# Kernel tuning notes

Measured on AMD Instinct MI355X. Metric: run time of the kernel, lower is better.

## Reference

```python
import jax, jax.numpy as jnp
import numpy as np

B, I, H = 8192, 1024, 1024


def setup_inputs() -> dict:
    key = jax.random.key(0)
    k1, k2, k3, k4, k5 = jax.random.split(key, 5)
    bound_in = 1.0 / np.sqrt(I)
    return {
        "input": jax.random.normal(k1, (B, I), dtype=jnp.float32),
        "weights": jax.random.uniform(k2, (4 * H, H + I), dtype=jnp.float32, minval=-bound_in, maxval=bound_in),
        "bias": jax.random.uniform(k3, (4 * H,), dtype=jnp.float32, minval=-bound_in, maxval=bound_in),
        "old_h": jax.random.normal(k4, (B, H), dtype=jnp.float32),
        "old_cell": jax.random.normal(k5, (B, H), dtype=jnp.float32),
    }


def reference(input, weights, bias, old_h, old_cell):
    # X = [old_h, input] matches weights = cat(recurrent_W, input_W, dim=1)
    X = jnp.concatenate([old_h, input], axis=1)            # [B, H+I]
    gates = jax.nn.sigmoid(X @ weights.T + bias)           # [B, 4H], all gates sigmoid
    in_g, out_g, z_g, f_g = jnp.split(gates, 4, axis=1)    # each [B, H]
    new_cell = old_cell * f_g + z_g - in_g                 # subtractive cell update
    new_h = jax.nn.sigmoid(new_cell) - out_g               # subtractive output
    return new_h, new_cell
```

## Files before the change

kernel.cpp:

```cpp
#include <hip/hip_runtime.h>
#include <hip/hip_bf16.h>

namespace {

constexpr int kB = 8192;
constexpr int kH = 1024;
constexpr int kK = 2048;
constexpr int kG = 4 * kH;

typedef float f32x4 __attribute__((ext_vector_type(4)));
typedef unsigned short u16x8 __attribute__((ext_vector_type(8)));
typedef unsigned short u16x4 __attribute__((ext_vector_type(4)));

__device__ __forceinline__ unsigned short f2bf(float f) {
  return __builtin_bit_cast(unsigned short, __float2bfloat16(f));
}
__device__ __forceinline__ float sigmoidf_(float x) {
  return 1.0f / (1.0f + __expf(-x));
}
__device__ __forceinline__ u16x4 pack4(const float4 v) {
  return u16x4{f2bf(v.x), f2bf(v.y), f2bf(v.z), f2bf(v.w)};
}

__global__ __launch_bounds__(256) void prep_pack(
    const float* __restrict__ input, const float* __restrict__ weights,
    const float* __restrict__ bias, const float* __restrict__ old_h,
    unsigned short* __restrict__ Aw, unsigned short* __restrict__ Ww,
    float* __restrict__ bias_i) {
  const int b = blockIdx.x;
  const int tid = threadIdx.x;

  if (b >= 768) {
    const int base = (b - 768) * 2048 + tid * 8;
    #pragma unroll
    for (int e = 0; e < 8; ++e) {
      const int j = base + e;
      bias_i[j] = bias[(j & 3) * kH + (j >> 2)];
    }
    return;
  }

  __shared__ unsigned short lbuf[128 * 280];

  const int wid = tid >> 6, lane = tid & 63;
  const bool isW = (b >= 512);
  const int blk = isW ? (b - 512) : b;
  const int rb = blk >> 3;
  const int kc = blk & 7;

  #pragma unroll
  for (int io = 0; io < 4; ++io) {
    float4 v[8];
    #pragma unroll
    for (int ii = 0; ii < 8; ++ii) {
      const int row = (io * 8 + ii) * 4 + wid;
      const float* base;
      if (!isW) {
        const long rowg = (long)rb * 128 + row;
        base = (kc < 4) ? (old_h + rowg * kH + kc * 256)
                        : (input + rowg * kH + (kc * 256 - kH));
      } else {
        const int j = rb * 128 + row;
        const int g = j & 3, h = j >> 2;
        base = weights + ((long)g * kH + h) * kK + kc * 256;
      }
      v[ii] = ((const float4*)base)[lane];
    }
    #pragma unroll
    for (int ii = 0; ii < 8; ++ii) {
      const int row = (io * 8 + ii) * 4 + wid;
      *(u16x4*)&lbuf[row * 280 + lane * 4] = pack4(v[ii]);
    }
  }
  __syncthreads();

  unsigned short* dst = (isW ? Ww : Aw) + ((long)rb * 32 + kc * 4) * 8192;
  #pragma unroll
  for (int it = 0; it < 16; ++it) {
    const int o = (it * 256 + tid) * 8;
    const int oo = o & 8191;
    const int tl = o >> 13;
    const int r15 = (oo >> 3) & 15;
    const int lh = (oo >> 7) & 3;
    const int kb = (oo >> 9) & 1;
    const int mb = oo >> 10;
    const int row = mb * 16 + r15;
    const int cs = tl * 64 + kb * 32 + lh * 8;
    *(u16x8*)(dst + o) = *(const u16x8*)&lbuf[row * 280 + cs];
  }
}

__global__ __launch_bounds__(512, 2) void sublstm_gemm(
    const unsigned short* __restrict__ Aw, const unsigned short* __restrict__ Ww,
    const float* __restrict__ bias_i, const float* __restrict__ old_cell,
    float* __restrict__ out) {

  __shared__ union SM {
    struct { unsigned short A0[16384]; unsigned short B0[16384];
             unsigned short A1[16384]; unsigned short B1[16384]; } t;
    float Gc[32][260];
  } sm;
  __shared__ float bias_s[256];

  const int tid  = threadIdx.x;
  const int lane = tid & 63;
  const int wid  = tid >> 6;
  const int wr   = wid >> 2;
  const int wc   = wid & 3;

  const int bid = blockIdx.x;
  const int swz = (bid & 7) * 64 + (bid >> 3);
  const int xc  = swz >> 6;
  const int i6  = swz & 63;
  const int bm  = (i6 >> 2) * 2 + (i6 & 1);
  const int hb  = xc * 2 + ((i6 >> 1) & 1);

  if (tid < 256) bias_s[tid] = bias_i[hb * 256 + tid];

  unsigned short* A0 = sm.t.A0; unsigned short* B0 = sm.t.B0;
  unsigned short* A1 = sm.t.A1; unsigned short* B1 = sm.t.B1;

  f32x4 acc[8][4];
  #pragma unroll
  for (int m = 0; m < 8; ++m)
    #pragma unroll
    for (int n = 0; n < 4; ++n)
      acc[m][n] = f32x4{0.f, 0.f, 0.f, 0.f};

#define STAGE(LA, LB, KT) do {                                                     \
    _Pragma("unroll")                                                              \
    for (int i_ = 0; i_ < 4; ++i_) {                                               \
      __builtin_amdgcn_global_load_lds(                                            \
          (const __attribute__((address_space(1))) unsigned int*)(                 \
              Aw + ((long)((2 * bm + (i_ >> 1)) * 32 + (KT))) * 8192               \
                 + (i_ & 1) * 4096 + tid * 8),                                     \
          (__attribute__((address_space(3))) unsigned int*)((LA) + i_ * 4096 + tid * 8), \
          16, 0, 0);                                                               \
      __builtin_amdgcn_global_load_lds(                                            \
          (const __attribute__((address_space(1))) unsigned int*)(                 \
              Ww + ((long)((2 * hb + (i_ >> 1)) * 32 + (KT))) * 8192               \
                 + (i_ & 1) * 4096 + tid * 8),                                     \
          (__attribute__((address_space(3))) unsigned int*)((LB) + i_ * 4096 + tid * 8), \
          16, 0, 0);                                                               \
    }                                                                              \
  } while (0)

#define COMPUTE(LA, LB) do {                                                       \
    _Pragma("unroll")                                                              \
    for (int kk_ = 0; kk_ < 2; ++kk_) {                                            \
      u16x8 bf_[4];                                                                \
      _Pragma("unroll")                                                            \
      for (int n_ = 0; n_ < 4; ++n_)                                               \
        bf_[n_] = *(const u16x8*)&(LB)[(wc >> 1) * 8192 + ((wc & 1) * 4 + n_) * 1024 \
                                        + kk_ * 512 + lane * 8];                   \
      _Pragma("unroll")                                                            \
      for (int m_ = 0; m_ < 8; ++m_) {                                             \
        u16x8 af_ = *(const u16x8*)&(LA)[wr * 8192 + m_ * 1024 + kk_ * 512 + lane * 8]; \
        _Pragma("unroll")                                                          \
        for (int n_ = 0; n_ < 4; ++n_)                                             \
          asm("v_mfma_f32_16x16x32_bf16 %0, %1, %2, %0"                            \
              : "+v"(acc[m_][n_]) : "v"(af_), "v"(bf_[n_]));                       \
      }                                                                            \
    }                                                                              \
  } while (0)

  STAGE(A0, B0, 0);
  __syncthreads();

  for (int kt = 0; kt + 2 < 32; kt += 2) {
    STAGE(A1, B1, kt + 1);
    COMPUTE(A0, B0);
    __syncthreads();
    STAGE(A0, B0, kt + 2);
    COMPUTE(A1, B1);
    __syncthreads();
  }
  STAGE(A1, B1, 31);

  float cnx[4];
  #pragma unroll
  for (int q = 0; q < 4; ++q) {
    const int grow = bm * 256 + q * 8 + wid;
    cnx[q] = old_cell[(long)grow * kH + hb * 64 + lane];
  }

  COMPUTE(A0, B0);
  __syncthreads();
  COMPUTE(A1, B1);

#undef STAGE
#undef COMPUTE

  float* out_h = out;
  float* out_c = out + (long)kB * kH;

  #pragma unroll
  for (int c = 0; c < 8; ++c) {
    const int wrc = c >> 2, mm = c & 3;
    __syncthreads();
    if (wr == wrc) {
      #pragma unroll
      for (int m2 = 0; m2 < 2; ++m2)
        #pragma unroll
        for (int n = 0; n < 4; ++n) {
          const int col = wc * 64 + n * 16 + (lane & 15);
          const int rb_ = m2 * 16 + (lane >> 4) * 4;
          #pragma unroll
          for (int j = 0; j < 4; ++j)
            sm.Gc[rb_ + j][col] = acc[mm * 2 + m2][n][j];
        }
    }
    __syncthreads();

    float cc[4];
    #pragma unroll
    for (int q = 0; q < 4; ++q) cc[q] = cnx[q];
    if (c < 7) {
      const int c2 = c + 1;
      #pragma unroll
      for (int q = 0; q < 4; ++q) {
        const int grow = bm * 256 + (c2 >> 2) * 128 + (c2 & 3) * 32 + q * 8 + wid;
        cnx[q] = old_cell[(long)grow * kH + hb * 64 + lane];
      }
    }

    #pragma unroll
    for (int q = 0; q < 4; ++q) {
      const int r = q * 8 + wid;
      const float4 gv = *(const float4*)&sm.Gc[r][lane * 4];
      const float4 bv = *(const float4*)&bias_s[lane * 4];
      const float gi = sigmoidf_(gv.x + bv.x);
      const float go = sigmoidf_(gv.y + bv.y);
      const float gz = sigmoidf_(gv.z + bv.z);
      const float gf = sigmoidf_(gv.w + bv.w);
      const int grow = bm * 256 + wrc * 128 + mm * 32 + r;
      const long off = (long)grow * kH + hb * 64 + lane;
      const float nc = cc[q] * gf + gz - gi;
      out_h[off] = sigmoidf_(nc) - go;
      out_c[off] = nc;
    }
  }
}

constexpr int FBM = 128, FBH = 32, FBN = 128, FBK = 32, FNKT = kK / FBK;

__device__ __forceinline__ u16x8 pack8f(const float4 v0, const float4 v1) {
  return u16x8{f2bf(v0.x), f2bf(v0.y), f2bf(v0.z), f2bf(v0.w),
               f2bf(v1.x), f2bf(v1.y), f2bf(v1.z), f2bf(v1.w)};
}

__global__ __launch_bounds__(256, 2) void sublstm_fused(
    const float* __restrict__ input, const float* __restrict__ weights,
    const float* __restrict__ bias, const float* __restrict__ old_h,
    const float* __restrict__ old_cell, float* __restrict__ out) {
  __shared__ unsigned short As[FBM][FBK + 8];
  __shared__ unsigned short Bs[FBN][FBK + 8];
  __shared__ float Gc[32][FBN + 4];

  const int tid = threadIdx.x, lane = tid & 63, wid = tid >> 6;
  const int wr = wid >> 1, wc = wid & 1;
  const int bid = blockIdx.x;
  const int bm = bid & 63, hh0 = (bid >> 6) * FBH;

  const int ra = tid >> 1, ca = (tid & 1) << 4;
  const long arow = (long)bm * FBM + ra;
  const int wrow = (ra >> 5) * kH + hh0 + (ra & 31);
  const float* abase_h = old_h + arow * kH + ca;
  const float* abase_x = input + arow * kH + ca - kH;
  const float* wbase = weights + (long)wrow * kK + ca;

  const int fr = lane & 15, ks = (lane >> 4) << 3;
  f32x4 acc[4][4];
  #pragma unroll
  for (int m = 0; m < 4; ++m)
    #pragma unroll
    for (int n = 0; n < 4; ++n) acc[m][n] = f32x4{0.f, 0.f, 0.f, 0.f};

  float4 a0, a1, a2, a3, b0, b1, b2, b3;
  {
    const float4* ap4 = (const float4*)abase_h;
    const float4* wp4 = (const float4*)wbase;
    a0 = ap4[0]; a1 = ap4[1]; a2 = ap4[2]; a3 = ap4[3];
    b0 = wp4[0]; b1 = wp4[1]; b2 = wp4[2]; b3 = wp4[3];
  }
  for (int kt = 0; kt < FNKT; ++kt) {
    u16x8 pa0 = pack8f(a0, a1), pa1 = pack8f(a2, a3);
    u16x8 pb0 = pack8f(b0, b1), pb1 = pack8f(b2, b3);
    __syncthreads();
    *(u16x8*)&As[ra][ca] = pa0; *(u16x8*)&As[ra][ca + 8] = pa1;
    *(u16x8*)&Bs[ra][ca] = pb0; *(u16x8*)&Bs[ra][ca + 8] = pb1;
    __syncthreads();
    if (kt + 1 < FNKT) {
      const int k0n = (kt + 1) * FBK;
      const float* ap = (k0n < kH) ? (abase_h + k0n) : (abase_x + k0n);
      const float4* ap4 = (const float4*)ap;
      const float4* wp4 = (const float4*)(wbase + k0n);
      a0 = ap4[0]; a1 = ap4[1]; a2 = ap4[2]; a3 = ap4[3];
      b0 = wp4[0]; b1 = wp4[1]; b2 = wp4[2]; b3 = wp4[3];
    }
    u16x8 af[4], bfv[4];
    #pragma unroll
    for (int m = 0; m < 4; ++m) af[m] = *(const u16x8*)&As[wr * 64 + m * 16 + fr][ks];
    #pragma unroll
    for (int n = 0; n < 4; ++n) bfv[n] = *(const u16x8*)&Bs[wc * 64 + n * 16 + fr][ks];
    #pragma unroll
    for (int m = 0; m < 4; ++m)
      #pragma unroll
      for (int n = 0; n < 4; ++n)
        asm("v_mfma_f32_16x16x32_bf16 %0, %1, %2, %0"
            : "+v"(acc[m][n]) : "v"(af[m]), "v"(bfv[n]));
  }
  float* out_h = out;
  float* out_c = out + (long)kB * kH;
  #pragma unroll
  for (int m = 0; m < 4; ++m) {
    __syncthreads();
    #pragma unroll
    for (int n = 0; n < 4; ++n) {
      const int col = wc * 64 + n * 16 + fr;
      #pragma unroll
      for (int j = 0; j < 4; ++j)
        Gc[wr * 16 + (lane >> 4) * 4 + j][col] = acc[m][n][j];
    }
    __syncthreads();
    #pragma unroll
    for (int q = 0; q < 4; ++q) {
      const int idx = tid + (q << 8);
      const int r = idx >> 5, h = idx & 31;
      const int hg = hh0 + h;
      const float gi = sigmoidf_(Gc[r][h] + bias[hg]);
      const float go = sigmoidf_(Gc[r][32 + h] + bias[kH + hg]);
      const float gz = sigmoidf_(Gc[r][64 + h] + bias[2 * kH + hg]);
      const float gf = sigmoidf_(Gc[r][96 + h] + bias[3 * kH + hg]);
      const int grow = bm * FBM + (r >> 4) * 64 + m * 16 + (r & 15);
      const long off = (long)grow * kH + hg;
      const float oc = old_cell[off];
      const float nc = oc * gf + gz - gi;
      out_h[off] = sigmoidf_(nc) - go;
      out_c[off] = nc;
    }
  }
}

}

extern "C" void kernel_launch(void* const* d_in, const int* in_sizes, int n_in,
                              void* d_out, int out_size, void* d_ws, size_t ws_size,
                              hipStream_t stream) {
  const float* input    = (const float*)d_in[0];
  const float* weights  = (const float*)d_in[1];
  const float* bias     = (const float*)d_in[2];
  const float* old_h    = (const float*)d_in[3];
  const float* old_cell = (const float*)d_in[4];
  float* out = (float*)d_out;

  const size_t needA = (size_t)kB * kK * 2;
  const size_t needW = (size_t)kG * kK * 2;
  const size_t needBias = (size_t)kG * 4;

  if (ws_size >= needA + needW + needBias) {
    unsigned short* Aw = (unsigned short*)d_ws;
    unsigned short* Ww = (unsigned short*)((char*)d_ws + needA);
    float* bias_i = (float*)((char*)d_ws + needA + needW);
    prep_pack<<<dim3(770), dim3(256), 0, stream>>>(input, weights, bias, old_h,
                                                   Aw, Ww, bias_i);
    sublstm_gemm<<<dim3(512), dim3(512), 0, stream>>>(Aw, Ww, bias_i, old_cell, out);
  } else {
    sublstm_fused<<<dim3(2048), dim3(256), 0, stream>>>(input, weights, bias, old_h,
                                                        old_cell, out);
  }
}
```

Before: 317.1 us.

## Deepen GEMM K pipeline to four half-size LDS stages with vmcnt waits

Splits each 64-wide K tile into two half tiles and rotates four LDS buffers, keeping three loads in flight instead of one. Uses explicit vmcnt waits with raw s_barrier in place of __syncthreads, and raises wave priority around the MFMA block. The aim is to hide global-to-LDS latency better in the bf16 GEMM. The cost is twice as many barriers per unit of K, and correctness now depends on the hand-counted vmcnt values.

```diff
diff --git a/kernel.cpp b/kernel.cpp
--- a/kernel.cpp
+++ b/kernel.cpp
@@ -96,8 +96,7 @@
     float* __restrict__ out) {
 
   __shared__ union SM {
-    struct { unsigned short A0[16384]; unsigned short B0[16384];
-             unsigned short A1[16384]; unsigned short B1[16384]; } t;
+    unsigned short buf[4][16384];
     float Gc[32][260];
   } sm;
   __shared__ float bias_s[256];
@@ -115,10 +114,12 @@
   const int bm  = (i6 >> 2) * 2 + (i6 & 1);
   const int hb  = xc * 2 + ((i6 >> 1) & 1);
 
-  if (tid < 256) bias_s[tid] = bias_i[hb * 256 + tid];
-
-  unsigned short* A0 = sm.t.A0; unsigned short* B0 = sm.t.B0;
-  unsigned short* A1 = sm.t.A1; unsigned short* B1 = sm.t.B1;
+  bias_s[tid & 255] = bias_i[hb * 256 + (tid & 255)];
+
+  const int soff = (tid >> 6) * 1024 + (tid & 63) * 8;
+  const int doff = tid * 8;
+  const int aoff = wr * 4096 + lane * 8;
+  const int bboff = (wc >> 1) * 4096 + (wc & 1) * 2048 + lane * 8;
 
   f32x4 acc[8][4];
   #pragma unroll
@@ -127,55 +128,57 @@
     for (int n = 0; n < 4; ++n)
       acc[m][n] = f32x4{0.f, 0.f, 0.f, 0.f};
 
-#define STAGE(LA, LB, KT) do {                                                     \
+#define BAR() __builtin_amdgcn_s_barrier()
+#define VMCNT(N) asm volatile("s_waitcnt vmcnt(" #N ")" ::: "memory")
+
+#define STAGE(J, T) do {                                                           \
     _Pragma("unroll")                                                              \
-    for (int i_ = 0; i_ < 4; ++i_) {                                               \
+    for (int h_ = 0; h_ < 2; ++h_) {                                               \
       __builtin_amdgcn_global_load_lds(                                            \
           (const __attribute__((address_space(1))) unsigned int*)(                 \
-              Aw + ((long)((2 * bm + (i_ >> 1)) * 32 + (KT))) * 8192               \
-                 + (i_ & 1) * 4096 + tid * 8),                                     \
-          (__attribute__((address_space(3))) unsigned int*)((LA) + i_ * 4096 + tid * 8), \
+              Aw + ((long)((2 * bm + h_) * 32 + ((T) >> 1))) * 8192                \
+                 + ((T) & 1) * 512 + soff),                                        \
+          (__attribute__((address_space(3))) unsigned int*)(&sm.buf[J][h_ * 4096 + doff]), \
           16, 0, 0);                                                               \
       __builtin_amdgcn_global_load_lds(                                            \
           (const __attribute__((address_space(1))) unsigned int*)(                 \
-              Ww + ((long)((2 * hb + (i_ >> 1)) * 32 + (KT))) * 8192               \
-                 + (i_ & 1) * 4096 + tid * 8),                                     \
-          (__attribute__((address_space(3))) unsigned int*)((LB) + i_ * 4096 + tid * 8), \
+              Ww + ((long)((2 * hb + h_) * 32 + ((T) >> 1))) * 8192                \
+                 + ((T) & 1) * 512 + soff),                                        \
+          (__attribute__((address_space(3))) unsigned int*)(&sm.buf[J][8192 + h_ * 4096 + doff]), \
           16, 0, 0);                                                               \
     }                                                                              \
   } while (0)
 
-#define COMPUTE(LA, LB) do {                                                       \
+#define COMPUTE(J) do {                                                            \
+    u16x8 bf_[4];                                                                  \
     _Pragma("unroll")                                                              \
-    for (int kk_ = 0; kk_ < 2; ++kk_) {                                            \
-      u16x8 bf_[4];                                                                \
+    for (int n_ = 0; n_ < 4; ++n_)                                                 \
+      bf_[n_] = *(const u16x8*)&sm.buf[J][8192 + bboff + n_ * 512];                \
+    __builtin_amdgcn_s_setprio(1);                                                 \
+    _Pragma("unroll")                                                              \
+    for (int m_ = 0; m_ < 8; ++m_) {                                               \
+      u16x8 af_ = *(const u16x8*)&sm.buf[J][aoff + m_ * 512];                      \
       _Pragma("unroll")                                                            \
       for (int n_ = 0; n_ < 4; ++n_)                                               \
-        bf_[n_] = *(const u16x8*)&(LB)[(wc >> 1) * 8192 + ((wc & 1) * 4 + n_) * 1024 \
-                                        + kk_ * 512 + lane * 8];                   \
-      _Pragma("unroll")                                                            \
-      for (int m_ = 0; m_ < 8; ++m_) {                                             \
-        u16x8 af_ = *(const u16x8*)&(LA)[wr * 8192 + m_ * 1024 + kk_ * 512 + lane * 8]; \
-        _Pragma("unroll")                                                          \
-        for (int n_ = 0; n_ < 4; ++n_)                                             \
-          asm("v_mfma_f32_16x16x32_bf16 %0, %1, %2, %0"                            \
-              : "+v"(acc[m_][n_]) : "v"(af_), "v"(bf_[n_]));                       \
-      }                                                                            \
+        asm("v_mfma_f32_16x16x32_bf16 %0, %1, %2, %0"                              \
+            : "+v"(acc[m_][n_]) : "v"(af_), "v"(bf_[n_]));                         \
     }                                                                              \
+    __builtin_amdgcn_s_setprio(0);                                                 \
   } while (0)
 
-  STAGE(A0, B0, 0);
-  __syncthreads();
-
-  for (int kt = 0; kt + 2 < 32; kt += 2) {
-    STAGE(A1, B1, kt + 1);
-    COMPUTE(A0, B0);
-    __syncthreads();
-    STAGE(A0, B0, kt + 2);
-    COMPUTE(A1, B1);
-    __syncthreads();
-  }
-  STAGE(A1, B1, 31);
+  STAGE(0, 0); STAGE(1, 1); STAGE(2, 2);
+
+  for (int i = 0; i < 15; ++i) {
+    const int t = i * 4;
+    VMCNT(8); BAR(); COMPUTE(0); BAR(); STAGE(3, t + 3);
+    VMCNT(8); BAR(); COMPUTE(1); BAR(); STAGE(0, t + 4);
+    VMCNT(8); BAR(); COMPUTE(2); BAR(); STAGE(1, t + 5);
+    VMCNT(8); BAR(); COMPUTE(3); BAR(); STAGE(2, t + 6);
+  }
+  VMCNT(8); BAR(); COMPUTE(0); BAR(); STAGE(3, 63);
+  VMCNT(8); BAR(); COMPUTE(1); BAR();
+  VMCNT(4); BAR(); COMPUTE(2); BAR();
+  VMCNT(0); BAR();
 
   float cnx[4];
   #pragma unroll
@@ -184,12 +187,12 @@
     cnx[q] = old_cell[(long)grow * kH + hb * 64 + lane];
   }
 
-  COMPUTE(A0, B0);
-  __syncthreads();
-  COMPUTE(A1, B1);
+  COMPUTE(3);
 
 #undef STAGE
 #undef COMPUTE
+#undef VMCNT
+#undef BAR
 
   float* out_h = out;
   float* out_c = out + (long)kB * kH;
```

New measurement: 433.8 us. 36.8% more time.
